# Kernel tuning notes

Hardware: AMD Instinct MI355X
Metric: run time of the kernel (lower is better)

## Reference

```python
import jax, jax.numpy as jnp
import numpy as np

B, S, D, E, F = 2, 2048, 1024, 8, 4096


def setup_inputs() -> dict:
    key = jax.random.key(0)
    k1, k2, k3, k4 = jax.random.split(key, 4)
    x = jax.random.normal(k1, (B, S, D), dtype=jnp.float32)
    gate_w = jax.random.normal(k2, (E, D), dtype=jnp.float32) * 0.02
    w1 = jax.random.normal(k3, (E, D, F), dtype=jnp.float32) * 0.02
    w2 = jax.random.normal(k4, (E, F, D), dtype=jnp.float32) * 0.02
    return {"x": x, "gate_w": gate_w, "w1": w1, "w2": w2}


def reference(x, gate_w, w1, w2):
    b, s, d = x.shape
    n_experts = w1.shape[0]
    tokens = x.reshape(-1, d)                      # (T, D)
    logits = tokens @ gate_w.T                     # (T, E) router (Linear, no bias)
    expert_ids = jnp.argmax(logits, axis=-1)       # top-1 routing (T,)
    dispatch = jax.nn.one_hot(expert_ids, n_experts, dtype=tokens.dtype)  # (T, E)
    # dense all-experts reference of the grouped GEMM: h_e = tokens @ w1[e]
    h = jnp.einsum('td,edf->etf', tokens, w1)      # (E, T, F)
    h = jax.nn.gelu(h, approximate=False)          # torch F.gelu default = exact erf
    out_e = jnp.einsum('etf,efd->etd', h, w2)      # (E, T, D)
    # scatter back: each token takes exactly its assigned expert's output
    out = jnp.einsum('etd,te->td', out_e, dispatch)
    return out.reshape(b, s, d)
```

## Files before the change

### kernel.cpp

```cpp
#include <hip/hip_runtime.h>
#include <math.h>

#define T_TOK 4096
#define D_DIM 1024
#define E_EXP 8
#define F_DIM 4096
#define BM 128
#define BN 128
#define BK 32
#define LDK 40
#define MAX_TILES 40
#define KSPLIT 4

typedef __attribute__((ext_vector_type(8))) short short8;
typedef __attribute__((ext_vector_type(4))) float float4v;

__device__ __forceinline__ short f2b(float f) {
    union { float f; unsigned u; } v; v.f = f;
    unsigned r = v.u + 0x7fffu + ((v.u >> 16) & 1u);
    return (short)(r >> 16);
}

__device__ __forceinline__ void gll16(const short* g, short* l) {
    __builtin_amdgcn_global_load_lds((const __attribute__((address_space(1))) unsigned*)g,
                                     (__attribute__((address_space(3))) unsigned*)l, 16, 0, 0);
}

__global__ void router_kernel(const float* __restrict__ x, const float* __restrict__ gw,
                              int* __restrict__ eid, int* __restrict__ rnk,
                              int* __restrict__ counts) {
    int lane = threadIdx.x & 63;
    int wave = threadIdx.x >> 6;
    int t = blockIdx.x * 4 + wave;
    const float* xr = x + (size_t)t * D_DIM;
    float p[E_EXP];
#pragma unroll
    for (int e = 0; e < E_EXP; ++e) p[e] = 0.f;
#pragma unroll
    for (int i = 0; i < D_DIM / 64; ++i) {
        float v = xr[lane + 64 * i];
#pragma unroll
        for (int e = 0; e < E_EXP; ++e)
            p[e] = fmaf(v, gw[e * D_DIM + lane + 64 * i], p[e]);
    }
#pragma unroll
    for (int off = 32; off > 0; off >>= 1) {
#pragma unroll
        for (int e = 0; e < E_EXP; ++e) p[e] += __shfl_down(p[e], off, 64);
    }
    if (lane == 0) {
        int best = 0; float bv = p[0];
#pragma unroll
        for (int e = 1; e < E_EXP; ++e) if (p[e] > bv) { bv = p[e]; best = e; }
        eid[t] = best;
        rnk[t] = atomicAdd(&counts[best], 1);
    }
}

__global__ void prefix_kernel(const int* __restrict__ counts, int* __restrict__ offsets,
                              int* __restrict__ tmap) {
    int off = 0;
    offsets[0] = 0;
    int nt = 0;
    for (int e = 0; e < E_EXP; ++e) {
        int c = counts[e];
        for (int m0 = 0; m0 < c; m0 += BM) {
            tmap[nt * 3 + 0] = e;
            tmap[nt * 3 + 1] = off + m0;
            tmap[nt * 3 + 2] = (c - m0 < BM) ? (c - m0) : BM;
            ++nt;
        }
        off += c;
        offsets[e + 1] = off;
    }
    for (; nt < MAX_TILES; ++nt) tmap[nt * 3 + 2] = 0;
}

__global__ void scatter_kernel(const int* __restrict__ eid, const int* __restrict__ rnk,
                               const int* __restrict__ offsets, int* __restrict__ sorted) {
    int t = blockIdx.x * 256 + threadIdx.x;
    sorted[offsets[eid[t]] + rnk[t]] = t;
}

__global__ __launch_bounds__(256) void cvt_x_kernel(const float* __restrict__ x,
                                                    short* __restrict__ xb) {
    size_t base = ((size_t)blockIdx.x * 256 + threadIdx.x) * 16;
    float4v f0 = *(const float4v*)(x + base);
    float4v f1 = *(const float4v*)(x + base + 4);
    float4v f2 = *(const float4v*)(x + base + 8);
    float4v f3 = *(const float4v*)(x + base + 12);
    short8 s0, s1;
#pragma unroll
    for (int c = 0; c < 4; ++c) {
        s0[c] = f2b(f0[c]); s0[4 + c] = f2b(f1[c]);
        s1[c] = f2b(f2[c]); s1[4 + c] = f2b(f3[c]);
    }
    *(short8*)(xb + base) = s0;
    *(short8*)(xb + base + 8) = s1;
}

__global__ __launch_bounds__(256) void tconv_kernel(const float* __restrict__ in,
                                                    short* __restrict__ outp, int R, int C) {
    __shared__ short t[64][72];
    size_t slab = (size_t)R * C;
    const float* ip = in + (size_t)blockIdx.z * slab + (size_t)(blockIdx.y * 64) * C + blockIdx.x * 64;
    short* op = outp + (size_t)blockIdx.z * slab + (size_t)(blockIdx.x * 64) * R + blockIdx.y * 64;
    int tid = threadIdx.x;
    int r = tid >> 2, c4 = (tid & 3) * 16;
    const float* p = ip + (size_t)r * C + c4;
    float4v f0 = *(const float4v*)(p);
    float4v f1 = *(const float4v*)(p + 4);
    float4v f2 = *(const float4v*)(p + 8);
    float4v f3 = *(const float4v*)(p + 12);
#pragma unroll
    for (int j = 0; j < 4; ++j) {
        t[c4 + j][r]      = f2b(f0[j]);
        t[c4 + 4 + j][r]  = f2b(f1[j]);
        t[c4 + 8 + j][r]  = f2b(f2[j]);
        t[c4 + 12 + j][r] = f2b(f3[j]);
    }
    __syncthreads();
    short* q = op + (size_t)r * R + c4;
    *(short8*)q       = *(const short8*)&t[r][c4];
    *(short8*)(q + 8) = *(const short8*)&t[r][c4 + 8];
}

__global__ __launch_bounds__(256) void gemm1_bf16(const short* __restrict__ xb,
                                                  const short* __restrict__ w1b,
                                                  const int* __restrict__ sorted,
                                                  const int* __restrict__ tmap,
                                                  short* __restrict__ hbuf) {
    __shared__ short As[BM * BK];
    __shared__ short Bs[BN * BK];
    __shared__ int srow[BM];
    int mt = blockIdx.y;
    int m_count = tmap[mt * 3 + 2];
    if (m_count == 0) return;
    int e = tmap[mt * 3 + 0];
    int row0 = tmap[mt * 3 + 1];
    int n0 = blockIdx.x * BN;
    int tid = threadIdx.x;
    if (tid < BM) srow[tid] = sorted[row0 + (tid < m_count ? tid : m_count - 1)];
    __syncthreads();

    int lane = tid & 63, wave = tid >> 6;
    int wm = (wave & 1) * 64, wn = (wave >> 1) * 64;
    float4v acc[4][4];
#pragma unroll
    for (int i = 0; i < 4; ++i)
#pragma unroll
        for (int j = 0; j < 4; ++j) acc[i][j] = (float4v)(0.f);

    int r0 = wave * 16 + (lane >> 2);
    int r1 = r0 + 64;
    int p0 = (((lane & 3) ^ ((r0 >> 1) & 3)) * 8);
    int p1 = (((lane & 3) ^ ((r1 >> 1) & 3)) * 8);
    const short* ag0 = xb + (size_t)srow[r0] * D_DIM + p0;
    const short* ag1 = xb + (size_t)srow[r1] * D_DIM + p1;
    const short* wbase = w1b + (size_t)e * D_DIM * F_DIM;
    const short* bg0 = wbase + (size_t)(n0 + r0) * D_DIM + p0;
    const short* bg1 = wbase + (size_t)(n0 + r1) * D_DIM + p1;
    short* lA0 = As + wave * 512;
    short* lA1 = As + wave * 512 + 2048;
    short* lB0 = Bs + wave * 512;
    short* lB1 = Bs + wave * 512 + 2048;

    int rfa = lane & 15;
    int clog = lane >> 4;

    for (int k0 = 0; k0 < D_DIM; k0 += BK) {
        gll16(ag0 + k0, lA0);
        gll16(ag1 + k0, lA1);
        gll16(bg0 + k0, lB0);
        gll16(bg1 + k0, lB1);
        __syncthreads();
        short8 af[4], bfr[4];
#pragma unroll
        for (int i = 0; i < 4; ++i) {
            int row = wm + i * 16 + rfa;
            af[i] = *(const short8*)(&As[row * BK + ((clog ^ ((row >> 1) & 3)) * 8)]);
        }
#pragma unroll
        for (int j = 0; j < 4; ++j) {
            int row = wn + j * 16 + rfa;
            bfr[j] = *(const short8*)(&Bs[row * BK + ((clog ^ ((row >> 1) & 3)) * 8)]);
        }
#pragma unroll
        for (int i = 0; i < 4; ++i)
#pragma unroll
            for (int j = 0; j < 4; ++j)
                acc[i][j] = __builtin_amdgcn_mfma_f32_16x16x32_bf16(af[i], bfr[j], acc[i][j], 0, 0, 0);
        __syncthreads();
    }
    int rbase = (lane >> 4) * 4;
    int cbase = lane & 15;
#pragma unroll
    for (int i = 0; i < 4; ++i) {
#pragma unroll
        for (int r = 0; r < 4; ++r) {
            int row = wm + i * 16 + rbase + r;
            if (row < m_count) {
                short* hp = hbuf + (size_t)(row0 + row) * F_DIM + n0 + wn + cbase;
#pragma unroll
                for (int j = 0; j < 4; ++j) {
                    float s = acc[i][j][r];
                    float g = 0.5f * s * (1.f + erff(s * 0.70710678118f));
                    hp[j * 16] = f2b(g);
                }
            }
        }
    }
}

__global__ __launch_bounds__(256) void gemm2_bf16(const short* __restrict__ hbuf,
                                                  const short* __restrict__ w2b,
                                                  const int* __restrict__ sorted,
                                                  const int* __restrict__ tmap,
                                                  float* __restrict__ out) {
    __shared__ short As[BM * BK];
    __shared__ short Bs[BN * BK];
    __shared__ int srow[BM];
    int mt = blockIdx.y;
    int m_count = tmap[mt * 3 + 2];
    if (m_count == 0) return;
    int e = tmap[mt * 3 + 0];
    int row0 = tmap[mt * 3 + 1];
    int n0 = blockIdx.x * BN;
    int ks0 = blockIdx.z * (F_DIM / KSPLIT);
    int tid = threadIdx.x;
    if (tid < BM) srow[tid] = sorted[row0 + (tid < m_count ? tid : m_count - 1)];
    __syncthreads();

    int lane = tid & 63, wave = tid >> 6;
    int wm = (wave & 1) * 64, wn = (wave >> 1) * 64;
    float4v acc[4][4];
#pragma unroll
    for (int i = 0; i < 4; ++i)
#pragma unroll
        for (int j = 0; j < 4; ++j) acc[i][j] = (float4v)(0.f);

    int r0 = wave * 16 + (lane >> 2);
    int r1 = r0 + 64;
    int p0 = (((lane & 3) ^ ((r0 >> 1) & 3)) * 8);
    int p1 = (((lane & 3) ^ ((r1 >> 1) & 3)) * 8);
    int cr0 = r0 < m_count ? r0 : m_count - 1;
    int cr1 = r1 < m_count ? r1 : m_count - 1;
    const short* ag0 = hbuf + (size_t)(row0 + cr0) * F_DIM + ks0 + p0;
    const short* ag1 = hbuf + (size_t)(row0 + cr1) * F_DIM + ks0 + p1;
    const short* wbase = w2b + (size_t)e * F_DIM * D_DIM;
    const short* bg0 = wbase + (size_t)(n0 + r0) * F_DIM + ks0 + p0;
    const short* bg1 = wbase + (size_t)(n0 + r1) * F_DIM + ks0 + p1;
    short* lA0 = As + wave * 512;
    short* lA1 = As + wave * 512 + 2048;
    short* lB0 = Bs + wave * 512;
    short* lB1 = Bs + wave * 512 + 2048;

    int rfa = lane & 15;
    int clog = lane >> 4;

    for (int k0 = 0; k0 < F_DIM / KSPLIT; k0 += BK) {
        gll16(ag0 + k0, lA0);
        gll16(ag1 + k0, lA1);
        gll16(bg0 + k0, lB0);
        gll16(bg1 + k0, lB1);
        __syncthreads();
        short8 af[4], bfr[4];
#pragma unroll
        for (int i = 0; i < 4; ++i) {
            int row = wm + i * 16 + rfa;
            af[i] = *(const short8*)(&As[row * BK + ((clog ^ ((row >> 1) & 3)) * 8)]);
        }
#pragma unroll
        for (int j = 0; j < 4; ++j) {
            int row = wn + j * 16 + rfa;
            bfr[j] = *(const short8*)(&Bs[row * BK + ((clog ^ ((row >> 1) & 3)) * 8)]);
        }
#pragma unroll
        for (int i = 0; i < 4; ++i)
#pragma unroll
            for (int j = 0; j < 4; ++j)
                acc[i][j] = __builtin_amdgcn_mfma_f32_16x16x32_bf16(af[i], bfr[j], acc[i][j], 0, 0, 0);
        __syncthreads();
    }
    int rbase = (lane >> 4) * 4;
    int cbase = lane & 15;
#pragma unroll
    for (int i = 0; i < 4; ++i) {
#pragma unroll
        for (int r = 0; r < 4; ++r) {
            int row = wm + i * 16 + rbase + r;
            if (row < m_count) {
                float* op = out + (size_t)srow[row] * D_DIM + n0 + wn + cbase;
#pragma unroll
                for (int j = 0; j < 4; ++j) atomicAdd(op + j * 16, acc[i][j][r]);
            }
        }
    }
}

__global__ __launch_bounds__(256) void gemm1_kernel(const float* __restrict__ x,
                                                    const float* __restrict__ w1,
                                                    const int* __restrict__ sorted,
                                                    const int* __restrict__ tmap,
                                                    short* __restrict__ hbuf) {
    __shared__ short As[BM * LDK];
    __shared__ short Bs[BN * LDK];
    __shared__ int srow[BM];
    int mt = blockIdx.y;
    int m_count = tmap[mt * 3 + 2];
    if (m_count == 0) return;
    int e = tmap[mt * 3 + 0];
    int row0 = tmap[mt * 3 + 1];
    int n0 = blockIdx.x * BN;
    int tid = threadIdx.x;
    if (tid < BM) srow[tid] = sorted[row0 + (tid < m_count ? tid : m_count - 1)];
    __syncthreads();

    int lane = tid & 63, wave = tid >> 6;
    int wm = (wave & 1) * 64, wn = (wave >> 1) * 64;
    float4v acc[4][4];
#pragma unroll
    for (int i = 0; i < 4; ++i)
#pragma unroll
        for (int j = 0; j < 4; ++j) acc[i][j] = (float4v)(0.f);

    int ar = tid >> 1;
    int ac = (tid & 1) * 16;
    int bn = tid & 127;
    int bq = (tid >> 7) * 16;
    const float* abase = x + (size_t)srow[ar] * D_DIM + ac;
    const float* bbase = w1 + (size_t)e * D_DIM * F_DIM + (size_t)bq * F_DIM + (n0 + bn);

    for (int k0 = 0; k0 < D_DIM; k0 += BK) {
        {
            const float* ap = abase + k0;
            float4v f0 = *(const float4v*)(ap);
            float4v f1 = *(const float4v*)(ap + 4);
            float4v f2 = *(const float4v*)(ap + 8);
            float4v f3 = *(const float4v*)(ap + 12);
            short8 s0, s1;
#pragma unroll
            for (int c = 0; c < 4; ++c) {
                s0[c] = f2b(f0[c]); s0[4 + c] = f2b(f1[c]);
                s1[c] = f2b(f2[c]); s1[4 + c] = f2b(f3[c]);
            }
            *(short8*)(&As[ar * LDK + ac]) = s0;
            *(short8*)(&As[ar * LDK + ac + 8]) = s1;
        }
        {
            const float* bp = bbase + (size_t)k0 * F_DIM;
            float v[16];
#pragma unroll
            for (int j = 0; j < 16; ++j) v[j] = bp[(size_t)j * F_DIM];
            short8 s0, s1;
#pragma unroll
            for (int j = 0; j < 8; ++j) { s0[j] = f2b(v[j]); s1[j] = f2b(v[8 + j]); }
            *(short8*)(&Bs[bn * LDK + bq]) = s0;
            *(short8*)(&Bs[bn * LDK + bq + 8]) = s1;
        }
        __syncthreads();
        short8 af[4], bfr[4];
#pragma unroll
        for (int i = 0; i < 4; ++i)
            af[i] = *(const short8*)(&As[(wm + i * 16 + (lane & 15)) * LDK + (lane >> 4) * 8]);
#pragma unroll
        for (int j = 0; j < 4; ++j)
            bfr[j] = *(const short8*)(&Bs[(wn + j * 16 + (lane & 15)) * LDK + (lane >> 4) * 8]);
#pragma unroll
        for (int i = 0; i < 4; ++i)
#pragma unroll
            for (int j = 0; j < 4; ++j)
                acc[i][j] = __builtin_amdgcn_mfma_f32_16x16x32_bf16(af[i], bfr[j], acc[i][j], 0, 0, 0);
        __syncthreads();
    }
    int rbase = (lane >> 4) * 4;
    int cbase = lane & 15;
#pragma unroll
    for (int i = 0; i < 4; ++i) {
#pragma unroll
        for (int r = 0; r < 4; ++r) {
            int row = wm + i * 16 + rbase + r;
            if (row < m_count) {
                short* hp = hbuf + (size_t)(row0 + row) * F_DIM + n0 + wn + cbase;
#pragma unroll
                for (int j = 0; j < 4; ++j) {
                    float s = acc[i][j][r];
                    float g = 0.5f * s * (1.f + erff(s * 0.70710678118f));
                    hp[j * 16] = f2b(g);
                }
            }
        }
    }
}

__global__ __launch_bounds__(256) void gemm2_kernel(const short* __restrict__ hbuf,
                                                    const float* __restrict__ w2,
                                                    const int* __restrict__ sorted,
                                                    const int* __restrict__ tmap,
                                                    float* __restrict__ out) {
    __shared__ short As[BM * LDK];
    __shared__ short Bs[BN * LDK];
    __shared__ int srow[BM];
    int mt = blockIdx.y;
    int m_count = tmap[mt * 3 + 2];
    if (m_count == 0) return;
    int e = tmap[mt * 3 + 0];
    int row0 = tmap[mt * 3 + 1];
    int n0 = blockIdx.x * BN;
    int tid = threadIdx.x;
    if (tid < BM) srow[tid] = sorted[row0 + (tid < m_count ? tid : m_count - 1)];
    __syncthreads();

    int lane = tid & 63, wave = tid >> 6;
    int wm = (wave & 1) * 64, wn = (wave >> 1) * 64;
    float4v acc[4][4];
#pragma unroll
    for (int i = 0; i < 4; ++i)
#pragma unroll
        for (int j = 0; j < 4; ++j) acc[i][j] = (float4v)(0.f);

    int ar = tid >> 1;
    int ac = (tid & 1) * 16;
    int bn = tid & 127;
    int bq = (tid >> 7) * 16;
    int arc = ar < m_count ? ar : m_count - 1;
    const short* abase = hbuf + (size_t)(row0 + arc) * F_DIM + ac;
    const float* bbase = w2 + (size_t)e * F_DIM * D_DIM + (size_t)bq * D_DIM + (n0 + bn);

    for (int k0 = 0; k0 < F_DIM; k0 += BK) {
        {
            const short* ap = abase + k0;
            *(short8*)(&As[ar * LDK + ac]) = *(const short8*)(ap);
            *(short8*)(&As[ar * LDK + ac + 8]) = *(const short8*)(ap + 8);
        }
        {
            const float* bp = bbase + (size_t)k0 * D_DIM;
            float v[16];
#pragma unroll
            for (int j = 0; j < 16; ++j) v[j] = bp[(size_t)j * D_DIM];
            short8 s0, s1;
#pragma unroll
            for (int j = 0; j < 8; ++j) { s0[j] = f2b(v[j]); s1[j] = f2b(v[8 + j]); }
            *(short8*)(&Bs[bn * LDK + bq]) = s0;
            *(short8*)(&Bs[bn * LDK + bq + 8]) = s1;
        }
        __syncthreads();
        short8 af[4], bfr[4];
#pragma unroll
        for (int i = 0; i < 4; ++i)
            af[i] = *(const short8*)(&As[(wm + i * 16 + (lane & 15)) * LDK + (lane >> 4) * 8]);
#pragma unroll
        for (int j = 0; j < 4; ++j)
            bfr[j] = *(const short8*)(&Bs[(wn + j * 16 + (lane & 15)) * LDK + (lane >> 4) * 8]);
#pragma unroll
        for (int i = 0; i < 4; ++i)
#pragma unroll
            for (int j = 0; j < 4; ++j)
                acc[i][j] = __builtin_amdgcn_mfma_f32_16x16x32_bf16(af[i], bfr[j], acc[i][j], 0, 0, 0);
        __syncthreads();
    }
    int rbase = (lane >> 4) * 4;
    int cbase = lane & 15;
#pragma unroll
    for (int i = 0; i < 4; ++i) {
#pragma unroll
        for (int r = 0; r < 4; ++r) {
            int row = wm + i * 16 + rbase + r;
            if (row < m_count) {
                float* op = out + (size_t)srow[row] * D_DIM + n0 + wn + cbase;
#pragma unroll
                for (int j = 0; j < 4; ++j) op[j * 16] = acc[i][j][r];
            }
        }
    }
}

extern "C" void kernel_launch(void* const* d_in, const int* in_sizes, int n_in,
                              void* d_out, int out_size, void* d_ws, size_t ws_size,
                              hipStream_t stream) {
    const float* x  = (const float*)d_in[0];
    const float* gw = (const float*)d_in[1];
    const float* w1 = (const float*)d_in[2];
    const float* w2 = (const float*)d_in[3];
    float* out = (float*)d_out;
    char* ws = (char*)d_ws;

    int* counts  = (int*)(ws);
    int* offsets = (int*)(ws + 64);
    int* tmap    = (int*)(ws + 128);
    int* eid     = (int*)(ws + 1024);
    int* rnk     = (int*)(ws + 17408);
    int* sorted  = (int*)(ws + 33792);
    short* hbuf  = (short*)(ws + 51200);

    const size_t HB  = 33554432ull;
    const size_t XB  = 8388608ull;
    const size_t WB  = 67108864ull;
    short* xb  = (short*)(ws + 51200 + HB);
    short* w1b = (short*)(ws + 51200 + HB + XB);
    short* w2b = (short*)(ws + 51200 + HB + XB + WB);
    const size_t need = 51200ull + HB + XB + 2ull * WB;
    bool fast = ws_size >= need;

    hipMemsetAsync(counts, 0, 32, stream);
    router_kernel<<<T_TOK / 4, 256, 0, stream>>>(x, gw, eid, rnk, counts);

    if (fast) {
        hipMemsetAsync(out, 0, (size_t)T_TOK * D_DIM * 4, stream);
        cvt_x_kernel<<<T_TOK * D_DIM / (256 * 16), 256, 0, stream>>>(x, xb);
        tconv_kernel<<<dim3(F_DIM / 64, D_DIM / 64, E_EXP), 256, 0, stream>>>(w1, w1b, D_DIM, F_DIM);
        tconv_kernel<<<dim3(D_DIM / 64, F_DIM / 64, E_EXP), 256, 0, stream>>>(w2, w2b, F_DIM, D_DIM);
    }

    prefix_kernel<<<1, 1, 0, stream>>>(counts, offsets, tmap);
    scatter_kernel<<<T_TOK / 256, 256, 0, stream>>>(eid, rnk, offsets, sorted);

    if (fast) {
        gemm1_bf16<<<dim3(F_DIM / BN, MAX_TILES), 256, 0, stream>>>(xb, w1b, sorted, tmap, hbuf);
        gemm2_bf16<<<dim3(D_DIM / BN, MAX_TILES, KSPLIT), 256, 0, stream>>>(hbuf, w2b, sorted, tmap, out);
    } else {
        gemm1_kernel<<<dim3(F_DIM / BN, MAX_TILES), 256, 0, stream>>>(x, w1, sorted, tmap, hbuf);
        gemm2_kernel<<<dim3(D_DIM / BN, MAX_TILES), 256, 0, stream>>>(hbuf, w2, sorted, tmap, out);
    }
}
```

Baseline: 554.5 us.

## Double-buffer GEMM LDS tiles, swizzle block order, fuse x conversion into router

Both grouped bf16 GEMMs now use two LDS buffers, so the global-to-LDS load for the next K step is issued before the MFMAs on the current one, overlapping memory with compute. Block indices are remapped with a stride swizzle to change the order tiles are scheduled, for cache locality. The separate x-to-bf16 conversion kernel is removed and folded into the router, which already reads x. The prefix kernel is parallelised across a wave. Together these cut launches and load stalls, at the cost of doubled LDS use per block.

```diff
diff --git a/kernel.cpp b/kernel.cpp
--- a/kernel.cpp
+++ b/kernel.cpp
@@ -27,6 +27,7 @@
 }
 
 __global__ void router_kernel(const float* __restrict__ x, const float* __restrict__ gw,
+                              short* __restrict__ xb,
                               int* __restrict__ eid, int* __restrict__ rnk,
                               int* __restrict__ counts) {
     int lane = threadIdx.x & 63;
@@ -39,6 +40,7 @@
 #pragma unroll
     for (int i = 0; i < D_DIM / 64; ++i) {
         float v = xr[lane + 64 * i];
+        if (xb) xb[(size_t)t * D_DIM + lane + 64 * i] = f2b(v);
 #pragma unroll
         for (int e = 0; e < E_EXP; ++e)
             p[e] = fmaf(v, gw[e * D_DIM + lane + 64 * i], p[e]);
@@ -59,44 +61,40 @@
 
 __global__ void prefix_kernel(const int* __restrict__ counts, int* __restrict__ offsets,
                               int* __restrict__ tmap) {
-    int off = 0;
-    offsets[0] = 0;
-    int nt = 0;
-    for (int e = 0; e < E_EXP; ++e) {
-        int c = counts[e];
-        for (int m0 = 0; m0 < c; m0 += BM) {
-            tmap[nt * 3 + 0] = e;
-            tmap[nt * 3 + 1] = off + m0;
-            tmap[nt * 3 + 2] = (c - m0 < BM) ? (c - m0) : BM;
-            ++nt;
-        }
-        off += c;
-        offsets[e + 1] = off;
-    }
-    for (; nt < MAX_TILES; ++nt) tmap[nt * 3 + 2] = 0;
+    __shared__ int cnt[E_EXP], off[E_EXP + 1], tp[E_EXP + 1];
+    int lane = threadIdx.x;
+    if (lane < E_EXP) cnt[lane] = counts[lane];
+    __syncthreads();
+    if (lane == 0) {
+        int o = 0, tv = 0;
+        off[0] = 0; tp[0] = 0;
+        for (int e = 0; e < E_EXP; ++e) {
+            o += cnt[e];
+            tv += (cnt[e] + BM - 1) / BM;
+            off[e + 1] = o; tp[e + 1] = tv;
+        }
+    }
+    __syncthreads();
+    if (lane < E_EXP + 1) offsets[lane] = off[lane];
+    if (lane < MAX_TILES) {
+        int e = 0;
+        while (e < E_EXP && tp[e + 1] <= lane) ++e;
+        if (e < E_EXP) {
+            int m0 = (lane - tp[e]) * BM;
+            int c = cnt[e];
+            tmap[lane * 3 + 0] = e;
+            tmap[lane * 3 + 1] = off[e] + m0;
+            tmap[lane * 3 + 2] = (c - m0 < BM) ? (c - m0) : BM;
+        } else {
+            tmap[lane * 3 + 2] = 0;
+        }
+    }
 }
 
 __global__ void scatter_kernel(const int* __restrict__ eid, const int* __restrict__ rnk,
                                const int* __restrict__ offsets, int* __restrict__ sorted) {
     int t = blockIdx.x * 256 + threadIdx.x;
     sorted[offsets[eid[t]] + rnk[t]] = t;
-}
-
-__global__ __launch_bounds__(256) void cvt_x_kernel(const float* __restrict__ x,
-                                                    short* __restrict__ xb) {
-    size_t base = ((size_t)blockIdx.x * 256 + threadIdx.x) * 16;
-    float4v f0 = *(const float4v*)(x + base);
-    float4v f1 = *(const float4v*)(x + base + 4);
-    float4v f2 = *(const float4v*)(x + base + 8);
-    float4v f3 = *(const float4v*)(x + base + 12);
-    short8 s0, s1;
-#pragma unroll
-    for (int c = 0; c < 4; ++c) {
-        s0[c] = f2b(f0[c]); s0[4 + c] = f2b(f1[c]);
-        s1[c] = f2b(f2[c]); s1[4 + c] = f2b(f3[c]);
-    }
-    *(short8*)(xb + base) = s0;
-    *(short8*)(xb + base + 8) = s1;
 }
 
 __global__ __launch_bounds__(256) void tconv_kernel(const float* __restrict__ in,
@@ -130,15 +128,18 @@
                                                   const int* __restrict__ sorted,
                                                   const int* __restrict__ tmap,
                                                   short* __restrict__ hbuf) {
-    __shared__ short As[BM * BK];
-    __shared__ short Bs[BN * BK];
+    __shared__ short As[2][BM * BK];
+    __shared__ short Bs[2][BN * BK];
     __shared__ int srow[BM];
-    int mt = blockIdx.y;
+    int flat = blockIdx.y * 32 + blockIdx.x;
+    int swz = (flat & 7) * 160 + (flat >> 3);
+    int bx = swz & 31;
+    int mt = swz >> 5;
     int m_count = tmap[mt * 3 + 2];
     if (m_count == 0) return;
     int e = tmap[mt * 3 + 0];
     int row0 = tmap[mt * 3 + 1];
-    int n0 = blockIdx.x * BN;
+    int n0 = bx * BN;
     int tid = threadIdx.x;
     if (tid < BM) srow[tid] = sorted[row0 + (tid < m_count ? tid : m_count - 1)];
     __syncthreads();
@@ -153,44 +154,54 @@
 
     int r0 = wave * 16 + (lane >> 2);
     int r1 = r0 + 64;
-    int p0 = (((lane & 3) ^ ((r0 >> 1) & 3)) * 8);
-    int p1 = (((lane & 3) ^ ((r1 >> 1) & 3)) * 8);
+    int p0 = ((lane & 3) ^ ((r0 >> 1) & 3)) * 8;
+    int p1 = ((lane & 3) ^ ((r1 >> 1) & 3)) * 8;
     const short* ag0 = xb + (size_t)srow[r0] * D_DIM + p0;
     const short* ag1 = xb + (size_t)srow[r1] * D_DIM + p1;
-    const short* wbase = w1b + (size_t)e * D_DIM * F_DIM;
-    const short* bg0 = wbase + (size_t)(n0 + r0) * D_DIM + p0;
-    const short* bg1 = wbase + (size_t)(n0 + r1) * D_DIM + p1;
-    short* lA0 = As + wave * 512;
-    short* lA1 = As + wave * 512 + 2048;
-    short* lB0 = Bs + wave * 512;
-    short* lB1 = Bs + wave * 512 + 2048;
+    const short* wb = w1b + (size_t)e * D_DIM * F_DIM;
+    const short* bg0 = wb + (size_t)(n0 + r0) * D_DIM + p0;
+    const short* bg1 = wb + (size_t)(n0 + r1) * D_DIM + p1;
+    int lofs = wave * 512;
 
     int rfa = lane & 15;
     int clog = lane >> 4;
-
-    for (int k0 = 0; k0 < D_DIM; k0 += BK) {
-        gll16(ag0 + k0, lA0);
-        gll16(ag1 + k0, lA1);
-        gll16(bg0 + k0, lB0);
-        gll16(bg1 + k0, lB1);
-        __syncthreads();
+    int aoff[4], boff[4];
+#pragma unroll
+    for (int i = 0; i < 4; ++i) {
+        int rowa = wm + i * 16 + rfa;
+        aoff[i] = rowa * BK + ((clog ^ ((rowa >> 1) & 3)) * 8);
+        int rowb = wn + i * 16 + rfa;
+        boff[i] = rowb * BK + ((clog ^ ((rowb >> 1) & 3)) * 8);
+    }
+
+    gll16(ag0, &As[0][lofs]);
+    gll16(ag1, &As[0][lofs + 2048]);
+    gll16(bg0, &Bs[0][lofs]);
+    gll16(bg1, &Bs[0][lofs + 2048]);
+    __syncthreads();
+
+    const int NT = D_DIM / BK;
+    int cur = 0;
+    for (int t = 0; t < NT; ++t) {
+        if (t + 1 < NT) {
+            int kn = (t + 1) * BK;
+            gll16(ag0 + kn, &As[cur ^ 1][lofs]);
+            gll16(ag1 + kn, &As[cur ^ 1][lofs + 2048]);
+            gll16(bg0 + kn, &Bs[cur ^ 1][lofs]);
+            gll16(bg1 + kn, &Bs[cur ^ 1][lofs + 2048]);
+        }
         short8 af[4], bfr[4];
 #pragma unroll
-        for (int i = 0; i < 4; ++i) {
-            int row = wm + i * 16 + rfa;
-            af[i] = *(const short8*)(&As[row * BK + ((clog ^ ((row >> 1) & 3)) * 8)]);
-        }
-#pragma unroll
-        for (int j = 0; j < 4; ++j) {
-            int row = wn + j * 16 + rfa;
-            bfr[j] = *(const short8*)(&Bs[row * BK + ((clog ^ ((row >> 1) & 3)) * 8)]);
-        }
+        for (int i = 0; i < 4; ++i) af[i] = *(const short8*)(&As[cur][aoff[i]]);
+#pragma unroll
+        for (int j = 0; j < 4; ++j) bfr[j] = *(const short8*)(&Bs[cur][boff[j]]);
 #pragma unroll
         for (int i = 0; i < 4; ++i)
 #pragma unroll
             for (int j = 0; j < 4; ++j)
                 acc[i][j] = __builtin_amdgcn_mfma_f32_16x16x32_bf16(af[i], bfr[j], acc[i][j], 0, 0, 0);
         __syncthreads();
+        cur ^= 1;
     }
     int rbase = (lane >> 4) * 4;
     int cbase = lane & 15;
@@ -217,16 +228,21 @@
                                                   const int* __restrict__ sorted,
                                                   const int* __restrict__ tmap,
                                                   float* __restrict__ out) {
-    __shared__ short As[BM * BK];
-    __shared__ short Bs[BN * BK];
+    __shared__ short As[2][BM * BK];
+    __shared__ short Bs[2][BN * BK];
     __shared__ int srow[BM];
-    int mt = blockIdx.y;
+    int flat = (blockIdx.z * 40 + blockIdx.y) * 8 + blockIdx.x;
+    int swz = (flat & 7) * 160 + (flat >> 3);
+    int bx = swz & 7;
+    int rest = swz >> 3;
+    int mt = rest % 40;
+    int kz = rest / 40;
     int m_count = tmap[mt * 3 + 2];
     if (m_count == 0) return;
     int e = tmap[mt * 3 + 0];
     int row0 = tmap[mt * 3 + 1];
-    int n0 = blockIdx.x * BN;
-    int ks0 = blockIdx.z * (F_DIM / KSPLIT);
+    int n0 = bx * BN;
+    int ks0 = kz * (F_DIM / KSPLIT);
     int tid = threadIdx.x;
     if (tid < BM) srow[tid] = sorted[row0 + (tid < m_count ? tid : m_count - 1)];
     __syncthreads();
@@ -241,46 +257,56 @@
 
     int r0 = wave * 16 + (lane >> 2);
     int r1 = r0 + 64;
-    int p0 = (((lane & 3) ^ ((r0 >> 1) & 3)) * 8);
-    int p1 = (((lane & 3) ^ ((r1 >> 1) & 3)) * 8);
+    int p0 = ((lane & 3) ^ ((r0 >> 1) & 3)) * 8;
+    int p1 = ((lane & 3) ^ ((r1 >> 1) & 3)) * 8;
     int cr0 = r0 < m_count ? r0 : m_count - 1;
     int cr1 = r1 < m_count ? r1 : m_count - 1;
     const short* ag0 = hbuf + (size_t)(row0 + cr0) * F_DIM + ks0 + p0;
     const short* ag1 = hbuf + (size_t)(row0 + cr1) * F_DIM + ks0 + p1;
-    const short* wbase = w2b + (size_t)e * F_DIM * D_DIM;
-    const short* bg0 = wbase + (size_t)(n0 + r0) * F_DIM + ks0 + p0;
-    const short* bg1 = wbase + (size_t)(n0 + r1) * F_DIM + ks0 + p1;
-    short* lA0 = As + wave * 512;
-    short* lA1 = As + wave * 512 + 2048;
-    short* lB0 = Bs + wave * 512;
-    short* lB1 = Bs + wave * 512 + 2048;
+    const short* wb = w2b + (size_t)e * F_DIM * D_DIM;
+    const short* bg0 = wb + (size_t)(n0 + r0) * F_DIM + ks0 + p0;
+    const short* bg1 = wb + (size_t)(n0 + r1) * F_DIM + ks0 + p1;
+    int lofs = wave * 512;
 
     int rfa = lane & 15;
     int clog = lane >> 4;
-
-    for (int k0 = 0; k0 < F_DIM / KSPLIT; k0 += BK) {
-        gll16(ag0 + k0, lA0);
-        gll16(ag1 + k0, lA1);
-        gll16(bg0 + k0, lB0);
-        gll16(bg1 + k0, lB1);
-        __syncthreads();
+    int aoff[4], boff[4];
+#pragma unroll
+    for (int i = 0; i < 4; ++i) {
+        int rowa = wm + i * 16 + rfa;
+        aoff[i] = rowa * BK + ((clog ^ ((rowa >> 1) & 3)) * 8);
+        int rowb = wn + i * 16 + rfa;
+        boff[i] = rowb * BK + ((clog ^ ((rowb >> 1) & 3)) * 8);
+    }
+
+    gll16(ag0, &As[0][lofs]);
+    gll16(ag1, &As[0][lofs + 2048]);
+    gll16(bg0, &Bs[0][lofs]);
+    gll16(bg1, &Bs[0][lofs + 2048]);
+    __syncthreads();
+
+    const int NT = (F_DIM / KSPLIT) / BK;
+    int cur = 0;
+    for (int t = 0; t < NT; ++t) {
+        if (t + 1 < NT) {
+            int kn = (t + 1) * BK;
+            gll16(ag0 + kn, &As[cur ^ 1][lofs]);
+            gll16(ag1 + kn, &As[cur ^ 1][lofs + 2048]);
+            gll16(bg0 + kn, &Bs[cur ^ 1][lofs]);
+            gll16(bg1 + kn, &Bs[cur ^ 1][lofs + 2048]);
+        }
         short8 af[4], bfr[4];
 #pragma unroll
-        for (int i = 0; i < 4; ++i) {
-            int row = wm + i * 16 + rfa;
-            af[i] = *(const short8*)(&As[row * BK + ((clog ^ ((row >> 1) & 3)) * 8)]);
-        }
-#pragma unroll
-        for (int j = 0; j < 4; ++j) {
-            int row = wn + j * 16 + rfa;
-            bfr[j] = *(const short8*)(&Bs[row * BK + ((clog ^ ((row >> 1) & 3)) * 8)]);
-        }
+        for (int i = 0; i < 4; ++i) af[i] = *(const short8*)(&As[cur][aoff[i]]);
+#pragma unroll
+        for (int j = 0; j < 4; ++j) bfr[j] = *(const short8*)(&Bs[cur][boff[j]]);
 #pragma unroll
         for (int i = 0; i < 4; ++i)
 #pragma unroll
             for (int j = 0; j < 4; ++j)
                 acc[i][j] = __builtin_amdgcn_mfma_f32_16x16x32_bf16(af[i], bfr[j], acc[i][j], 0, 0, 0);
         __syncthreads();
+        cur ^= 1;
     }
     int rbase = (lane >> 4) * 4;
     int cbase = lane & 15;
@@ -503,16 +529,15 @@
     bool fast = ws_size >= need;
 
     hipMemsetAsync(counts, 0, 32, stream);
-    router_kernel<<<T_TOK / 4, 256, 0, stream>>>(x, gw, eid, rnk, counts);
+    router_kernel<<<T_TOK / 4, 256, 0, stream>>>(x, gw, fast ? xb : (short*)0, eid, rnk, counts);
 
     if (fast) {
         hipMemsetAsync(out, 0, (size_t)T_TOK * D_DIM * 4, stream);
-        cvt_x_kernel<<<T_TOK * D_DIM / (256 * 16), 256, 0, stream>>>(x, xb);
         tconv_kernel<<<dim3(F_DIM / 64, D_DIM / 64, E_EXP), 256, 0, stream>>>(w1, w1b, D_DIM, F_DIM);
         tconv_kernel<<<dim3(D_DIM / 64, F_DIM / 64, E_EXP), 256, 0, stream>>>(w2, w2b, F_DIM, D_DIM);
     }
 
-    prefix_kernel<<<1, 1, 0, stream>>>(counts, offsets, tmap);
+    prefix_kernel<<<1, 64, 0, stream>>>(counts, offsets, tmap);
     scatter_kernel<<<T_TOK / 256, 256, 0, stream>>>(eid, rnk, offsets, sorted);
 
     if (fast) {
```

New measurement: 574.2 us. 3.6% more time.
